# Performance work log

Measured on AMD Instinct MI355X. Metric: run time of the kernel, lower is better.

## Reference

```python
import jax, jax.numpy as jnp
import numpy as np

C, H_HEADS, L_LEV, M_PTS = 256, 4, 3, 4
TAU0 = 1.0


def _ln(x, g, b, eps=1e-5):
    mu = x.mean(-1, keepdims=True)
    var = ((x - mu) ** 2).mean(-1, keepdims=True)
    return (x - mu) * jax.lax.rsqrt(var + eps) * g + b


def _grid_sample(v, grid):
    """Bilinear grid_sample, padding_mode='zeros', align_corners=True.
    v: [B,C,Hin,Win], grid: [B,N,2] (x,y) in [-1,1] -> [B,N,C]"""
    B, Cc, Hin, Win = v.shape
    x = (grid[..., 0] + 1.0) * 0.5 * (Win - 1)
    y = (grid[..., 1] + 1.0) * 0.5 * (Hin - 1)
    x0 = jnp.floor(x); y0 = jnp.floor(y)
    wx1 = x - x0; wy1 = y - y0
    x0i = x0.astype(jnp.int32); y0i = y0.astype(jnp.int32)
    vflat = v.reshape(B, Cc, Hin * Win).transpose(0, 2, 1)  # [B,HW,C]

    def tap(yi, xi, w):
        valid = ((xi >= 0) & (xi < Win) & (yi >= 0) & (yi < Hin)).astype(v.dtype)
        idx = jnp.clip(yi, 0, Hin - 1) * Win + jnp.clip(xi, 0, Win - 1)  # [B,N]
        g = jax.vmap(lambda vf, i: vf[i])(vflat, idx)  # [B,N,C]
        return g * (w * valid)[..., None]

    return (tap(y0i, x0i, (1 - wy1) * (1 - wx1))
            + tap(y0i, x0i + 1, (1 - wy1) * wx1)
            + tap(y0i + 1, x0i, wy1 * (1 - wx1))
            + tap(y0i + 1, x0i + 1, wy1 * wx1))


def setup_inputs() -> dict:
    key = jax.random.key(0)
    ks = jax.random.split(key, 32)
    B, Hq, Wq = 2, 64, 64
    cins = [256, 512, 1024]
    d = {
        'S':  jax.random.normal(ks[0], (B, C, Hq, Wq), jnp.float32),
        'f0': jax.random.normal(ks[1], (B, cins[0], 64, 64), jnp.float32),
        'f1': jax.random.normal(ks[2], (B, cins[1], 32, 32), jnp.float32),
        'f2': jax.random.normal(ks[3], (B, cins[2], 16, 16), jnp.float32),
        'sim': jax.random.uniform(ks[4], (B, 1, Hq, Wq), jnp.float32),
        # 1x1 conv value projections per level
        'vw0': jax.random.normal(ks[5], (C, cins[0]), jnp.float32) * 0.02,
        'vb0': jnp.zeros((C,), jnp.float32),
        'vw1': jax.random.normal(ks[6], (C, cins[1]), jnp.float32) * 0.02,
        'vb1': jnp.zeros((C,), jnp.float32),
        'vw2': jax.random.normal(ks[7], (C, cins[2]), jnp.float32) * 0.02,
        'vb2': jnp.zeros((C,), jnp.float32),
        'q_w': jax.random.normal(ks[8], (C, C), jnp.float32) * 0.02,
        'q_b': jnp.zeros((C,), jnp.float32),
        # offset/weight predictors (non-zero so sampling is nontrivial)
        'off_w': jax.random.normal(ks[9], (H_HEADS * L_LEV * M_PTS * 2, C), jnp.float32) * 0.01,
        'off_b': jnp.zeros((H_HEADS * L_LEV * M_PTS * 2,), jnp.float32),
        'wgt_w': jax.random.normal(ks[10], (H_HEADS * L_LEV * M_PTS, C), jnp.float32) * 0.02,
        'wgt_b': jnp.zeros((H_HEADS * L_LEV * M_PTS,), jnp.float32),
        'out_w': jax.random.normal(ks[11], (C, H_HEADS * C), jnp.float32) * 0.02,
        'out_b': jnp.zeros((C,), jnp.float32),
        'lnq_g': jnp.ones((C,), jnp.float32), 'lnq_b': jnp.zeros((C,), jnp.float32),
        'lno_g': jnp.ones((C,), jnp.float32), 'lno_b': jnp.zeros((C,), jnp.float32),
        'fc1_w': jax.random.normal(ks[12], (4 * C, C), jnp.float32) * 0.02,
        'fc1_b': jnp.zeros((4 * C,), jnp.float32),
        'fc2_w': jax.random.normal(ks[13], (C, 4 * C), jnp.float32) * 0.02,
        'fc2_b': jnp.zeros((C,), jnp.float32),
    }
    return d


def reference(S, f0, f1, f2, sim, vw0, vb0, vw1, vb1, vw2, vb2, q_w, q_b,
              off_w, off_b, wgt_w, wgt_b, out_w, out_b,
              lnq_g, lnq_b, lno_g, lno_b, fc1_w, fc1_b, fc2_w, fc2_b):
    B, Cc, Hq, Wq = S.shape
    Nq = Hq * Wq
    S_seq = S.reshape(B, Cc, Nq).transpose(0, 2, 1)  # [B,Nq,C]
    Q = _ln(S_seq @ q_w.T + q_b, lnq_g, lnq_b)

    # reference points in [0,1], (x,y)
    ys = jnp.linspace(0.5 / Hq, 1 - 0.5 / Hq, Hq)
    xs = jnp.linspace(0.5 / Wq, 1 - 0.5 / Wq, Wq)
    yy, xx = jnp.meshgrid(ys, xs, indexing='ij')
    ref = jnp.stack([xx, yy], axis=-1).reshape(1, Nq, 2)

    feats = [(f0, vw0, vb0), (f1, vw1, vb1), (f2, vw2, vb2)]
    V = [jnp.einsum('bchw,oc->bohw', f, w) + b[None, :, None, None] for f, w, b in feats]

    off = (Q @ off_w.T + off_b).reshape(B, Nq, H_HEADS, L_LEV, M_PTS, 2)
    wts = (Q @ wgt_w.T + wgt_b).reshape(B, Nq, H_HEADS, L_LEV, M_PTS)

    sim2 = sim[:, 0].reshape(B, Nq, 1)
    tau = TAU0 / (sim2 + 0.001)
    wts = wts / tau.reshape(B, Nq, 1, 1, 1)
    wts = jax.nn.softmax(wts.reshape(B, Nq, H_HEADS, L_LEV * M_PTS), axis=-1)
    wts = wts.reshape(B, Nq, H_HEADS, L_LEV, M_PTS)

    acc = jnp.zeros((B, Nq, H_HEADS, Cc), S.dtype)
    for l in range(L_LEV):
        g01 = ref.reshape(1, Nq, 1, 1, 2) + off[:, :, :, l]  # [B,Nq,H,M,2]
        g = jnp.clip(jnp.tanh(g01 * 2.0 - 1.0), -1.0, 1.0)
        samp = _grid_sample(V[l], g.reshape(B, Nq * H_HEADS * M_PTS, 2))
        samp = samp.reshape(B, Nq, H_HEADS, M_PTS, Cc)
        acc = acc + jnp.einsum('bqhmc,bqhm->bqhc', samp, wts[:, :, :, l])

    Y = acc.reshape(B, Nq, H_HEADS * Cc) @ out_w.T + out_b
    Z = _ln(S_seq + Y, lno_g, lno_b)
    h = jax.nn.gelu(Z @ fc1_w.T + fc1_b, approximate=False)
    Z = Z + (h @ fc2_w.T + fc2_b)
    return Z.transpose(0, 2, 1).reshape(B, Cc, Hq, Wq)
```

## Files before the change

kernel.cpp:

```cpp
#include <hip/hip_runtime.h>
#include <hip/hip_bf16.h>
#include <math.h>

#define NQ 4096
#define CC 256

typedef __attribute__((ext_vector_type(8))) short bfrag;
typedef __attribute__((ext_vector_type(4))) float ffrag;

__device__ inline unsigned short f2bf(float x) {
  __hip_bfloat16 h = __float2bfloat16(x);
  return *reinterpret_cast<unsigned short*>(&h);
}

__device__ inline void gload16(const void* g, void* l) {
  __builtin_amdgcn_global_load_lds(
      (const __attribute__((address_space(1))) void*)g,
      (__attribute__((address_space(3))) void*)l, 16, 0, 0);
}

__device__ void tr64(const float* __restrict__ src, float* __restrict__ dstf,
                     unsigned short* __restrict__ dstb, int Cin, int P,
                     int p0, int c0, int b, float (*t)[73]) {
  int tid = threadIdx.x;
  int rx = tid & 15, ry = tid >> 4;
  const float* Sb = src + (size_t)b * Cin * P + p0 + rx * 4;
  #pragma unroll
  for (int i = 0; i < 4; i++) {
    int r = ry + i * 16;
    float4 v = *(const float4*)(Sb + (size_t)(c0 + r) * P);
    t[r][rx * 4 + 0] = v.x; t[r][rx * 4 + 1] = v.y;
    t[r][rx * 4 + 2] = v.z; t[r][rx * 4 + 3] = v.w;
  }
  __syncthreads();
  size_t ob = (size_t)b * P * Cin;
  #pragma unroll
  for (int i = 0; i < 4; i++) {
    int pr = ry + i * 16;
    float x0 = t[rx * 4 + 0][pr], x1 = t[rx * 4 + 1][pr];
    float x2 = t[rx * 4 + 2][pr], x3 = t[rx * 4 + 3][pr];
    size_t idx = ob + (size_t)(p0 + pr) * Cin + c0 + rx * 4;
    if (dstf) { float4 f4 = make_float4(x0, x1, x2, x3); *(float4*)(dstf + idx) = f4; }
    ushort4 u4;
    u4.x = f2bf(x0); u4.y = f2bf(x1); u4.z = f2bf(x2); u4.w = f2bf(x3);
    *(ushort4*)(dstb + idx) = u4;
  }
}

__global__ __launch_bounds__(256)
void prep_all_k(const float* S, const float* f0, const float* f1, const float* f2,
                const float* q_w, const float* off_w, const float* wgt_w,
                const float* vw0, const float* vw1, const float* vw2,
                const float* out_w, const float* fc1_w, const float* fc2_w,
                const float* off_b, const float* wgt_b,
                float* Sseq, unsigned short* Sbf,
                unsigned short* Xf0, unsigned short* Xf1, unsigned short* Xf2,
                unsigned short* q_wb, unsigned short* owb,
                unsigned short* vw0b, unsigned short* vw1b, unsigned short* vw2b,
                unsigned short* out_wb, unsigned short* fc1_wb,
                unsigned short* fc2_wb, float* bias144) {
  __shared__ float t[64][73];
  int bid = blockIdx.x;
  if (bid < 512) {
    int l = bid;
    tr64(S, Sseq, Sbf, 256, 4096, (l & 63) * 64, ((l >> 6) & 3) * 64, l >> 8, t);
  } else if (bid < 1024) {
    int l = bid - 512;
    tr64(f0, nullptr, Xf0, 256, 4096, (l & 63) * 64, ((l >> 6) & 3) * 64, l >> 8, t);
  } else if (bid < 1280) {
    int l = bid - 1024;
    tr64(f1, nullptr, Xf1, 512, 1024, (l & 15) * 64, ((l >> 4) & 7) * 64, l >> 7, t);
  } else if (bid < 1408) {
    int l = bid - 1280;
    tr64(f2, nullptr, Xf2, 1024, 256, (l & 3) * 64, ((l >> 2) & 15) * 64, l >> 6, t);
  } else if (bid < 2688) {
    int i4 = (bid - 1408) * 256 + threadIdx.x;
    const float* src; unsigned short* dst;
    if (i4 < 16384)       { src = q_w;   dst = q_wb; }
    else if (i4 < 32768)  { i4 -= 16384;  src = vw0;   dst = vw0b; }
    else if (i4 < 65536)  { i4 -= 32768;  src = vw1;   dst = vw1b; }
    else if (i4 < 131072) { i4 -= 65536;  src = vw2;   dst = vw2b; }
    else if (i4 < 196608) { i4 -= 131072; src = out_w; dst = out_wb; }
    else if (i4 < 262144) { i4 -= 196608; src = fc1_w; dst = fc1_wb; }
    else                  { i4 -= 262144; src = fc2_w; dst = fc2_wb; }
    float4 v = ((const float4*)src)[i4];
    ushort4 u; u.x = f2bf(v.x); u.y = f2bf(v.y); u.z = f2bf(v.z); u.w = f2bf(v.w);
    ((ushort4*)dst)[i4] = u;
  } else {
    int e = (bid - 2688) * 256 + threadIdx.x;
    float v = (e < 24576) ? off_w[e] : (e < 36864 ? wgt_w[e - 24576] : 0.f);
    owb[e] = f2bf(v);
    if (e < 96) bias144[e] = off_b[e];
    else if (e < 144) bias144[e] = wgt_b[e - 96];
  }
}

template<int BM, int BN, int WM, int WN, int EPI>
__device__ __forceinline__ void gemm_body(
    const unsigned short* __restrict__ A, const unsigned short* __restrict__ B,
    const float* __restrict__ bias, float* __restrict__ outf,
    unsigned short* __restrict__ outb, int N, int K, int ldo,
    const float* __restrict__ Zres, float* __restrict__ outT,
    int m0, int n0, unsigned short* As, unsigned short* Bs) {
  constexpr int MI = BM / (WM * 16), NI = BN / (WN * 16);
  constexpr int TA = BM / 8, TB = BN / 8;
  constexpr int LBM = (BM == 32) ? 5 : (BM == 64) ? 6 : 7;
  constexpr int LBN = (BN == 64) ? 6 : (BN == 128) ? 7 : 8;
  int tid = threadIdx.x, wave = tid >> 6, lane = tid & 63;
  int quad = lane >> 4, l16 = lane & 15;
  int wm = wave / WN, wn = wave % WN;
  const int mbase = wm * (BM / WM), nbase = wn * (BN / WN);

  ffrag acc[MI][NI];
  #pragma unroll
  for (int i = 0; i < MI; i++)
    #pragma unroll
    for (int j = 0; j < NI; j++) acc[i][j] = (ffrag)0.f;

  for (int k0 = 0; k0 < K; k0 += 64) {
    __syncthreads();
    for (int t = wave; t < TA + TB; t += 4) {
      if (t < TA) {
        int s = t * 64 + lane;
        int kc = s >> LBM, r = s & (BM - 1);
        gload16(A + (size_t)(m0 + r) * K + k0 + kc * 8, (char*)As + t * 1024);
      } else {
        int s = (t - TA) * 64 + lane;
        int kc = s >> LBN, r = s & (BN - 1);
        gload16(B + (size_t)(n0 + r) * K + k0 + kc * 8, (char*)Bs + (t - TA) * 1024);
      }
    }
    __syncthreads();
    #pragma unroll
    for (int ks = 0; ks < 2; ks++) {
      bfrag af[MI], bf[NI];
      #pragma unroll
      for (int mi = 0; mi < MI; mi++)
        af[mi] = *(const bfrag*)(As + ((((ks * 4 + quad) << LBM) + mbase + mi * 16 + l16) << 3));
      #pragma unroll
      for (int ni = 0; ni < NI; ni++)
        bf[ni] = *(const bfrag*)(Bs + ((((ks * 4 + quad) << LBN) + nbase + ni * 16 + l16) << 3));
      #pragma unroll
      for (int mi = 0; mi < MI; mi++)
        #pragma unroll
        for (int ni = 0; ni < NI; ni++)
          acc[mi][ni] = __builtin_amdgcn_mfma_f32_16x16x32_bf16(
              af[mi], bf[ni], acc[mi][ni], 0, 0, 0);
    }
  }

  if (EPI == 2) {
    #pragma unroll
    for (int mi = 0; mi < MI; mi++) {
      int mrow = m0 + mbase + mi * 16 + quad * 4;
      int bb = mrow >> 12, q0 = mrow & (NQ - 1);
      #pragma unroll
      for (int ni = 0; ni < NI; ni++) {
        int n = n0 + nbase + ni * 16 + l16;
        float bv = bias[n];
        float4 v;
        v.x = acc[mi][ni][0] + bv + Zres[(size_t)(mrow + 0) * CC + n];
        v.y = acc[mi][ni][1] + bv + Zres[(size_t)(mrow + 1) * CC + n];
        v.z = acc[mi][ni][2] + bv + Zres[(size_t)(mrow + 2) * CC + n];
        v.w = acc[mi][ni][3] + bv + Zres[(size_t)(mrow + 3) * CC + n];
        *(float4*)(outT + ((size_t)(bb * CC + n)) * NQ + q0) = v;
      }
    }
  } else {
    #pragma unroll
    for (int mi = 0; mi < MI; mi++) {
      int mrow = m0 + mbase + mi * 16 + quad * 4;
      #pragma unroll
      for (int ni = 0; ni < NI; ni++) {
        int n = n0 + nbase + ni * 16 + l16;
        if (n < N) {
          float bv = bias[n];
          #pragma unroll
          for (int r = 0; r < 4; r++) {
            float v = acc[mi][ni][r] + bv;
            if (EPI == 1) {
              v = 0.5f * v * (1.f + erff(v * 0.70710678118654752f));
              outb[(size_t)(mrow + r) * ldo + n] = f2bf(v);
            } else if (EPI == 3) {
              outb[(size_t)(mrow + r) * ldo + n] = f2bf(v);
            } else {
              outf[(size_t)(mrow + r) * ldo + n] = v;
            }
          }
        }
      }
    }
  }
}

template<bool RES>
__device__ __forceinline__ void gemm_ln_body(
    const unsigned short* __restrict__ A, const unsigned short* __restrict__ B,
    const float* __restrict__ bias, const float* __restrict__ res,
    float* __restrict__ outf, unsigned short* __restrict__ outb,
    const float* __restrict__ g, const float* __restrict__ be,
    int K, int m0, char* sm) {
  unsigned short* As = (unsigned short*)sm;
  unsigned short* Bs = (unsigned short*)(sm + 4096);
  float* L = (float*)sm;

  int tid = threadIdx.x, wave = tid >> 6, lane = tid & 63;
  int quad = lane >> 4, l16 = lane & 15;

  ffrag acc[2][4];
  #pragma unroll
  for (int i = 0; i < 2; i++)
    #pragma unroll
    for (int j = 0; j < 4; j++) acc[i][j] = (ffrag)0.f;

  for (int k0 = 0; k0 < K; k0 += 64) {
    __syncthreads();
    for (int t = wave; t < 36; t += 4) {
      if (t < 4) {
        int s = t * 64 + lane;
        int kc = s >> 5, r = s & 31;
        gload16(A + (size_t)(m0 + r) * K + k0 + kc * 8, sm + t * 1024);
      } else {
        int s = (t - 4) * 64 + lane;
        int kc = s >> 8, r = s & 255;
        gload16(B + (size_t)r * K + k0 + kc * 8, sm + 4096 + (t - 4) * 1024);
      }
    }
    __syncthreads();
    #pragma unroll
    for (int ks = 0; ks < 2; ks++) {
      bfrag af[2], bf[4];
      #pragma unroll
      for (int mi = 0; mi < 2; mi++)
        af[mi] = *(const bfrag*)(As + ((((ks * 4 + quad) << 5) + mi * 16 + l16) << 3));
      #pragma unroll
      for (int ni = 0; ni < 4; ni++)
        bf[ni] = *(const bfrag*)(Bs + ((((ks * 4 + quad) << 8) + wave * 64 + ni * 16 + l16) << 3));
      #pragma unroll
      for (int mi = 0; mi < 2; mi++)
        #pragma unroll
        for (int ni = 0; ni < 4; ni++)
          acc[mi][ni] = __builtin_amdgcn_mfma_f32_16x16x32_bf16(
              af[mi], bf[ni], acc[mi][ni], 0, 0, 0);
    }
  }
  __syncthreads();

  #pragma unroll
  for (int mi = 0; mi < 2; mi++) {
    int row = mi * 16 + quad * 4;
    #pragma unroll
    for (int ni = 0; ni < 4; ni++) {
      int col = wave * 64 + ni * 16 + l16;
      float bv = bias[col];
      #pragma unroll
      for (int r = 0; r < 4; r++) {
        float v = acc[mi][ni][r] + bv;
        if (RES) v += res[(size_t)(m0 + row + r) * CC + col];
        L[(row + r) * 264 + col] = v;
      }
    }
  }
  __syncthreads();

  int row = tid >> 3, j = tid & 7;
  int seg = ((j + row) & 7) * 32;
  const float* Lr = L + row * 264 + seg;
  float s1 = 0.f, s2 = 0.f;
  #pragma unroll
  for (int i = 0; i < 8; i++) {
    float4 t4 = *(const float4*)(Lr + i * 4);
    s1 += t4.x + t4.y + t4.z + t4.w;
    s2 += t4.x * t4.x + t4.y * t4.y + t4.z * t4.z + t4.w * t4.w;
  }
  #pragma unroll
  for (int o = 1; o < 8; o <<= 1) {
    s1 += __shfl_xor(s1, o);
    s2 += __shfl_xor(s2, o);
  }
  float mu = s1 * (1.f / 256.f);
  float var = s2 * (1.f / 256.f) - mu * mu;
  float rs = rsqrtf(var + 1e-5f);
  int gm = m0 + row;
  #pragma unroll
  for (int i = 0; i < 8; i++) {
    int col = seg + i * 4;
    float4 t4 = *(const float4*)(Lr + i * 4);
    float4 gg = *(const float4*)(g + col);
    float4 bb4 = *(const float4*)(be + col);
    float4 y;
    y.x = (t4.x - mu) * rs * gg.x + bb4.x;
    y.y = (t4.y - mu) * rs * gg.y + bb4.y;
    y.z = (t4.z - mu) * rs * gg.z + bb4.z;
    y.w = (t4.w - mu) * rs * gg.w + bb4.w;
    ushort4 ub;
    ub.x = f2bf(y.x); ub.y = f2bf(y.y); ub.z = f2bf(y.z); ub.w = f2bf(y.w);
    *(ushort4*)(outb + (size_t)gm * CC + col) = ub;
    if (RES) *(float4*)(outf + (size_t)gm * CC + col) = y;
  }
}

__global__ __launch_bounds__(256)
void qv_k(const unsigned short* Sbf, const unsigned short* q_wb, const float* q_b,
          const float* lnq_g, const float* lnq_b, unsigned short* Qbf,
          const unsigned short* Xf0, const unsigned short* Xf1,
          const unsigned short* Xf2, const unsigned short* vw0b,
          const unsigned short* vw1b, const unsigned short* vw2b,
          const float* vb0, const float* vb1, const float* vb2,
          unsigned short* V0b, unsigned short* V1b, unsigned short* V2b) {
  __shared__ __attribute__((aligned(16))) char sm[36864];
  int bid = blockIdx.x;
  if (bid < 256) {
    gemm_ln_body<false>(Sbf, q_wb, q_b, nullptr, nullptr, Qbf,
                        lnq_g, lnq_b, 256, bid * 32, sm);
  } else {
    int lb = bid - 256;
    const unsigned short *A, *B; const float* bias; unsigned short* out; int K;
    if (lb < 256)      { A = Xf0; B = vw0b; bias = vb0; out = V0b; K = 256; }
    else if (lb < 320) { A = Xf1; B = vw1b; bias = vb1; out = V1b; K = 512;  lb -= 256; }
    else               { A = Xf2; B = vw2b; bias = vb2; out = V2b; K = 1024; lb -= 320; }
    int n0 = (lb & 1) * 128, m0 = (lb >> 1) * 64;
    gemm_body<64, 128, 2, 2, 3>(A, B, bias, nullptr, out, 256, K, 256,
                                nullptr, nullptr, m0, n0,
                                (unsigned short*)sm, (unsigned short*)(sm + 8192));
  }
}

__global__ __launch_bounds__(256)
void outln_k(const unsigned short* accbf, const unsigned short* out_wb,
             const float* out_b, const float* Sseq, float* Z,
             unsigned short* Zbf, const float* lno_g, const float* lno_b) {
  __shared__ __attribute__((aligned(16))) char sm[36864];
  gemm_ln_body<true>(accbf, out_wb, out_b, Sseq, Z, Zbf,
                     lno_g, lno_b, 1024, blockIdx.x * 32, sm);
}

__global__ __launch_bounds__(256)
void offwgt_k(const unsigned short* Qbf, const unsigned short* owb,
              const float* bias144, float* offwgt) {
  __shared__ __attribute__((aligned(16))) unsigned short As[4096];
  __shared__ __attribute__((aligned(16))) unsigned short Bs[8192];
  gemm_body<64, 128, 2, 2, 0>(Qbf, owb, bias144, offwgt, nullptr, 144, 256, 144,
                              nullptr, nullptr, blockIdx.y * 64, blockIdx.x * 128, As, Bs);
}

__global__ __launch_bounds__(256)
void fc1_k(const unsigned short* Zbf, const unsigned short* fc1_wb,
           const float* fc1_b, unsigned short* hbf) {
  __shared__ __attribute__((aligned(16))) unsigned short As[8192];
  __shared__ __attribute__((aligned(16))) unsigned short Bs[8192];
  gemm_body<128, 128, 2, 2, 1>(Zbf, fc1_wb, fc1_b, nullptr, hbf, 1024, 256, 1024,
                               nullptr, nullptr, blockIdx.y * 128, blockIdx.x * 128, As, Bs);
}

__global__ __launch_bounds__(256)
void fc2_k(const unsigned short* hbf, const unsigned short* fc2_wb,
           const float* fc2_b, const float* Z, float* outp) {
  __shared__ __attribute__((aligned(16))) unsigned short As[4096];
  __shared__ __attribute__((aligned(16))) unsigned short Bs[4096];
  gemm_body<64, 64, 2, 2, 2>(hbf, fc2_wb, fc2_b, nullptr, nullptr, 256, 1024, 256,
                             Z, outp, blockIdx.y * 64, blockIdx.x * 64, As, Bs);
}

__global__ __launch_bounds__(256)
void sample_k(const float* __restrict__ ow, const float* __restrict__ sim,
              const unsigned short* __restrict__ V0, const unsigned short* __restrict__ V1,
              const unsigned short* __restrict__ V2, unsigned short* __restrict__ acc) {
  int bn = blockIdx.x;
  int q = ((bn & 7) << 10) | (bn >> 3);
  int b = q >> 12, n = q & (NQ - 1);
  int tid = threadIdx.x, head = tid >> 6, lane = tid & 63;

  __shared__ float s_w[48];
  __shared__ int   s_xy[48][2];
  __shared__ float s_f[48][2];
  __shared__ int   s_off[192];
  __shared__ float s_twt[192];

  if (tid < 48) {
    int hh = tid / 12, pt = tid % 12, l = pt >> 2, mm = pt & 3;
    int oidx = (hh * 3 + l) * 4 + mm;
    float offx = ow[(size_t)q * 144 + oidx * 2 + 0];
    float offy = ow[(size_t)q * 144 + oidx * 2 + 1];
    float refx = ((n & 63) + 0.5f) * (1.f / 64.f);
    float refy = ((n >> 6) + 0.5f) * (1.f / 64.f);
    float gx = tanhf((refx + offx) * 2.f - 1.f);
    float gy = tanhf((refy + offy) * 2.f - 1.f);
    gx = fminf(1.f, fmaxf(-1.f, gx));
    gy = fminf(1.f, fmaxf(-1.f, gy));
    int Wl = 64 >> l;
    float x = (gx + 1.f) * 0.5f * (float)(Wl - 1);
    float y = (gy + 1.f) * 0.5f * (float)(Wl - 1);
    float x0 = floorf(x), y0 = floorf(y);
    s_xy[tid][0] = (int)x0;
    s_xy[tid][1] = (int)y0;
    s_f[tid][0] = x - x0;
    s_f[tid][1] = y - y0;
    s_w[tid] = ow[(size_t)q * 144 + 96 + oidx] * (sim[q] + 0.001f);
  }
  __syncthreads();
  if (tid < 4) {
    float mx = -1e30f;
    #pragma unroll
    for (int i = 0; i < 12; i++) mx = fmaxf(mx, s_w[tid * 12 + i]);
    float e[12], ssum = 0.f;
    #pragma unroll
    for (int i = 0; i < 12; i++) { e[i] = expf(s_w[tid * 12 + i] - mx); ssum += e[i]; }
    float inv = 1.f / ssum;
    #pragma unroll
    for (int i = 0; i < 12; i++) s_w[tid * 12 + i] = e[i] * inv;
  }
  __syncthreads();
  if (tid < 192) {
    int s = tid >> 2, tap = tid & 3;
    int l = (s % 12) >> 2;
    int Wl = 64 >> l;
    int X = s_xy[s][0] + (tap & 1), Y = s_xy[s][1] + (tap >> 1);
    bool valid = (X >= 0 && X < Wl && Y >= 0 && Y < Wl);
    float wx = (tap & 1) ? s_f[s][0] : 1.f - s_f[s][0];
    float wy = (tap >> 1) ? s_f[s][1] : 1.f - s_f[s][1];
    s_twt[tid] = valid ? s_w[s] * wx * wy : 0.f;
    int Xc = min(max(X, 0), Wl - 1), Yc = min(max(Y, 0), Wl - 1);
    s_off[tid] = (Yc * Wl + Xc) << 8;
  }
  __syncthreads();

  const unsigned short* B0 = V0 + (size_t)b * 4096 * CC;
  const unsigned short* B1 = V1 + (size_t)b * 1024 * CC;
  const unsigned short* B2 = V2 + (size_t)b * 256 * CC;
  int lane4 = lane * 4;
  float4 a = make_float4(0.f, 0.f, 0.f, 0.f);
  #pragma unroll
  for (int pt = 0; pt < 12; pt++) {
    const unsigned short* base = (pt < 4) ? B0 : (pt < 8) ? B1 : B2;
    int s = head * 12 + pt;
    #pragma unroll
    for (int tap = 0; tap < 4; tap++) {
      int off = s_off[s * 4 + tap];
      float w = s_twt[s * 4 + tap];
      const uint2 u = *(const uint2*)(base + off + lane4);
      a.x = fmaf(w, __uint_as_float(u.x << 16), a.x);
      a.y = fmaf(w, __uint_as_float(u.x & 0xffff0000u), a.y);
      a.z = fmaf(w, __uint_as_float(u.y << 16), a.z);
      a.w = fmaf(w, __uint_as_float(u.y & 0xffff0000u), a.w);
    }
  }
  ushort4 r;
  r.x = f2bf(a.x); r.y = f2bf(a.y); r.z = f2bf(a.z); r.w = f2bf(a.w);
  *(ushort4*)(acc + (size_t)q * 1024 + head * CC + lane4) = r;
}

extern "C" void kernel_launch(void* const* d_in, const int* in_sizes, int n_in,
                              void* d_out, int out_size, void* d_ws, size_t ws_size,
                              hipStream_t stream) {
  const float* S     = (const float*)d_in[0];
  const float* f0    = (const float*)d_in[1];
  const float* f1    = (const float*)d_in[2];
  const float* f2    = (const float*)d_in[3];
  const float* sim   = (const float*)d_in[4];
  const float* vw0   = (const float*)d_in[5];
  const float* vb0   = (const float*)d_in[6];
  const float* vw1   = (const float*)d_in[7];
  const float* vb1   = (const float*)d_in[8];
  const float* vw2   = (const float*)d_in[9];
  const float* vb2   = (const float*)d_in[10];
  const float* q_w   = (const float*)d_in[11];
  const float* q_b   = (const float*)d_in[12];
  const float* off_w = (const float*)d_in[13];
  const float* off_b = (const float*)d_in[14];
  const float* wgt_w = (const float*)d_in[15];
  const float* wgt_b = (const float*)d_in[16];
  const float* out_w = (const float*)d_in[17];
  const float* out_b = (const float*)d_in[18];
  const float* lnq_g = (const float*)d_in[19];
  const float* lnq_b = (const float*)d_in[20];
  const float* lno_g = (const float*)d_in[21];
  const float* lno_b = (const float*)d_in[22];
  const float* fc1_w = (const float*)d_in[23];
  const float* fc1_b = (const float*)d_in[24];
  const float* fc2_w = (const float*)d_in[25];
  const float* fc2_b = (const float*)d_in[26];

  char* p = (char*)d_ws;
  float* Sseq   = (float*)p; p += 8388608;
  float* Z      = (float*)p; p += 8388608;
  float* offwgt = (float*)p; p += 4718592;
  float* bias144 = (float*)p; p += 1024;
  unsigned short* Sbf   = (unsigned short*)p; p += 4194304;
  unsigned short* Qbf   = (unsigned short*)p; p += 4194304;
  unsigned short* accbf = (unsigned short*)p; p += 16777216;
  unsigned short* V0b   = (unsigned short*)p; p += 4194304;
  unsigned short* V1b   = (unsigned short*)p; p += 1048576;
  unsigned short* V2b   = (unsigned short*)p; p += 262144;
  unsigned short* q_wb   = (unsigned short*)p; p += 131072;
  unsigned short* owb    = (unsigned short*)p; p += 131072;
  unsigned short* vw0b   = (unsigned short*)p; p += 131072;
  unsigned short* vw1b   = (unsigned short*)p; p += 262144;
  unsigned short* vw2b   = (unsigned short*)p; p += 524288;
  unsigned short* out_wb = (unsigned short*)p; p += 524288;
  unsigned short* fc1_wb = (unsigned short*)p; p += 524288;
  unsigned short* fc2_wb = (unsigned short*)p; p += 524288;

  unsigned short* Xf0 = accbf;
  unsigned short* Xf1 = accbf + 2097152;
  unsigned short* Xf2 = accbf + 3145728;
  unsigned short* Zbf = Qbf;
  unsigned short* hbf = accbf;
  float* outp = (float*)d_out;

  prep_all_k<<<2944, 256, 0, stream>>>(S, f0, f1, f2, q_w, off_w, wgt_w,
      vw0, vw1, vw2, out_w, fc1_w, fc2_w, off_b, wgt_b,
      Sseq, Sbf, Xf0, Xf1, Xf2, q_wb, owb, vw0b, vw1b, vw2b, out_wb,
      fc1_wb, fc2_wb, bias144);

  qv_k<<<592, 256, 0, stream>>>(Sbf, q_wb, q_b, lnq_g, lnq_b, Qbf,
      Xf0, Xf1, Xf2, vw0b, vw1b, vw2b, vb0, vb1, vb2, V0b, V1b, V2b);

  offwgt_k<<<dim3(2, 128), 256, 0, stream>>>(Qbf, owb, bias144, offwgt);

  sample_k<<<8192, 256, 0, stream>>>(offwgt, sim, V0b, V1b, V2b, accbf);

  outln_k<<<256, 256, 0, stream>>>(accbf, out_wb, out_b, Sseq, Z, Zbf,
      lno_g, lno_b);

  fc1_k<<<dim3(8, 64), 256, 0, stream>>>(Zbf, fc1_wb, fc1_b, hbf);

  fc2_k<<<dim3(4, 128), 256, 0, stream>>>(hbf, fc2_wb, fc2_b, Z, outp);
}
```

Measured before the change: 296.1 us.

## Drop fp32 transposed S copy and widen sampler gathers to 16-byte loads

The prep kernel no longer writes a transposed fp32 copy of S. The out-projection LayerNorm epilogue now reads the residual straight from the original channel-major S layout with float4 loads across four consecutive queries. Separately, the sampling kernel has each half-wave gather 8 bf16 channels per tap with uint4 loads, splitting the taps between halves and combining them with a cross-half shuffle. This cuts per-lane load count and packs offset and weight into one LDS entry. The trade-off is strided residual reads in the epilogue and an extra shuffle reduction in the sampler.

```diff
diff --git a/kernel.cpp b/kernel.cpp
--- a/kernel.cpp
+++ b/kernel.cpp
@@ -19,7 +19,7 @@
       (__attribute__((address_space(3))) void*)l, 16, 0, 0);
 }
 
-__device__ void tr64(const float* __restrict__ src, float* __restrict__ dstf,
+__device__ void tr64(const float* __restrict__ src,
                      unsigned short* __restrict__ dstb, int Cin, int P,
                      int p0, int c0, int b, float (*t)[73]) {
   int tid = threadIdx.x;
@@ -40,7 +40,6 @@
     float x0 = t[rx * 4 + 0][pr], x1 = t[rx * 4 + 1][pr];
     float x2 = t[rx * 4 + 2][pr], x3 = t[rx * 4 + 3][pr];
     size_t idx = ob + (size_t)(p0 + pr) * Cin + c0 + rx * 4;
-    if (dstf) { float4 f4 = make_float4(x0, x1, x2, x3); *(float4*)(dstf + idx) = f4; }
     ushort4 u4;
     u4.x = f2bf(x0); u4.y = f2bf(x1); u4.z = f2bf(x2); u4.w = f2bf(x3);
     *(ushort4*)(dstb + idx) = u4;
@@ -53,7 +52,7 @@
                 const float* vw0, const float* vw1, const float* vw2,
                 const float* out_w, const float* fc1_w, const float* fc2_w,
                 const float* off_b, const float* wgt_b,
-                float* Sseq, unsigned short* Sbf,
+                unsigned short* Sbf,
                 unsigned short* Xf0, unsigned short* Xf1, unsigned short* Xf2,
                 unsigned short* q_wb, unsigned short* owb,
                 unsigned short* vw0b, unsigned short* vw1b, unsigned short* vw2b,
@@ -63,16 +62,16 @@
   int bid = blockIdx.x;
   if (bid < 512) {
     int l = bid;
-    tr64(S, Sseq, Sbf, 256, 4096, (l & 63) * 64, ((l >> 6) & 3) * 64, l >> 8, t);
+    tr64(S, Sbf, 256, 4096, (l & 63) * 64, ((l >> 6) & 3) * 64, l >> 8, t);
   } else if (bid < 1024) {
     int l = bid - 512;
-    tr64(f0, nullptr, Xf0, 256, 4096, (l & 63) * 64, ((l >> 6) & 3) * 64, l >> 8, t);
+    tr64(f0, Xf0, 256, 4096, (l & 63) * 64, ((l >> 6) & 3) * 64, l >> 8, t);
   } else if (bid < 1280) {
     int l = bid - 1024;
-    tr64(f1, nullptr, Xf1, 512, 1024, (l & 15) * 64, ((l >> 4) & 7) * 64, l >> 7, t);
+    tr64(f1, Xf1, 512, 1024, (l & 15) * 64, ((l >> 4) & 7) * 64, l >> 7, t);
   } else if (bid < 1408) {
     int l = bid - 1280;
-    tr64(f2, nullptr, Xf2, 1024, 256, (l & 3) * 64, ((l >> 2) & 15) * 64, l >> 6, t);
+    tr64(f2, Xf2, 1024, 256, (l & 3) * 64, ((l >> 2) & 15) * 64, l >> 6, t);
   } else if (bid < 2688) {
     int i4 = (bid - 1408) * 256 + threadIdx.x;
     const float* src; unsigned short* dst;
@@ -196,7 +195,7 @@
 template<bool RES>
 __device__ __forceinline__ void gemm_ln_body(
     const unsigned short* __restrict__ A, const unsigned short* __restrict__ B,
-    const float* __restrict__ bias, const float* __restrict__ res,
+    const float* __restrict__ bias, const float* __restrict__ Sraw,
     float* __restrict__ outf, unsigned short* __restrict__ outb,
     const float* __restrict__ g, const float* __restrict__ be,
     int K, int m0, char* sm) {
@@ -249,16 +248,18 @@
   #pragma unroll
   for (int mi = 0; mi < 2; mi++) {
     int row = mi * 16 + quad * 4;
+    int m = m0 + row;
+    int bb = m >> 12, q0 = m & (NQ - 1);
     #pragma unroll
     for (int ni = 0; ni < 4; ni++) {
       int col = wave * 64 + ni * 16 + l16;
       float bv = bias[col];
-      #pragma unroll
-      for (int r = 0; r < 4; r++) {
-        float v = acc[mi][ni][r] + bv;
-        if (RES) v += res[(size_t)(m0 + row + r) * CC + col];
-        L[(row + r) * 264 + col] = v;
-      }
+      float4 s4 = make_float4(0.f, 0.f, 0.f, 0.f);
+      if (RES) s4 = *(const float4*)(Sraw + ((size_t)(bb * CC + col)) * NQ + q0);
+      L[(row + 0) * 264 + col] = acc[mi][ni][0] + bv + s4.x;
+      L[(row + 1) * 264 + col] = acc[mi][ni][1] + bv + s4.y;
+      L[(row + 2) * 264 + col] = acc[mi][ni][2] + bv + s4.z;
+      L[(row + 3) * 264 + col] = acc[mi][ni][3] + bv + s4.w;
     }
   }
   __syncthreads();
@@ -328,10 +329,10 @@
 
 __global__ __launch_bounds__(256)
 void outln_k(const unsigned short* accbf, const unsigned short* out_wb,
-             const float* out_b, const float* Sseq, float* Z,
+             const float* out_b, const float* S, float* Z,
              unsigned short* Zbf, const float* lno_g, const float* lno_b) {
   __shared__ __attribute__((aligned(16))) char sm[36864];
-  gemm_ln_body<true>(accbf, out_wb, out_b, Sseq, Z, Zbf,
+  gemm_ln_body<true>(accbf, out_wb, out_b, S, Z, Zbf,
                      lno_g, lno_b, 1024, blockIdx.x * 32, sm);
 }
 
@@ -370,12 +371,12 @@
   int q = ((bn & 7) << 10) | (bn >> 3);
   int b = q >> 12, n = q & (NQ - 1);
   int tid = threadIdx.x, head = tid >> 6, lane = tid & 63;
+  int half = lane >> 5, l32 = lane & 31;
 
   __shared__ float s_w[48];
   __shared__ int   s_xy[48][2];
   __shared__ float s_f[48][2];
-  __shared__ int   s_off[192];
-  __shared__ float s_twt[192];
+  __shared__ uint2 s_ow[192];
 
   if (tid < 48) {
     int hh = tid / 12, pt = tid % 12, l = pt >> 2, mm = pt & 3;
@@ -419,35 +420,46 @@
     bool valid = (X >= 0 && X < Wl && Y >= 0 && Y < Wl);
     float wx = (tap & 1) ? s_f[s][0] : 1.f - s_f[s][0];
     float wy = (tap >> 1) ? s_f[s][1] : 1.f - s_f[s][1];
-    s_twt[tid] = valid ? s_w[s] * wx * wy : 0.f;
+    float twt = valid ? s_w[s] * wx * wy : 0.f;
     int Xc = min(max(X, 0), Wl - 1), Yc = min(max(Y, 0), Wl - 1);
-    s_off[tid] = (Yc * Wl + Xc) << 8;
+    s_ow[tid].x = (unsigned)((Yc * Wl + Xc) << 8);
+    s_ow[tid].y = __float_as_uint(twt);
   }
   __syncthreads();
 
   const unsigned short* B0 = V0 + (size_t)b * 4096 * CC;
   const unsigned short* B1 = V1 + (size_t)b * 1024 * CC;
   const unsigned short* B2 = V2 + (size_t)b * 256 * CC;
-  int lane4 = lane * 4;
-  float4 a = make_float4(0.f, 0.f, 0.f, 0.f);
-  #pragma unroll
-  for (int pt = 0; pt < 12; pt++) {
-    const unsigned short* base = (pt < 4) ? B0 : (pt < 8) ? B1 : B2;
-    int s = head * 12 + pt;
-    #pragma unroll
-    for (int tap = 0; tap < 4; tap++) {
-      int off = s_off[s * 4 + tap];
-      float w = s_twt[s * 4 + tap];
-      const uint2 u = *(const uint2*)(base + off + lane4);
-      a.x = fmaf(w, __uint_as_float(u.x << 16), a.x);
-      a.y = fmaf(w, __uint_as_float(u.x & 0xffff0000u), a.y);
-      a.z = fmaf(w, __uint_as_float(u.y << 16), a.z);
-      a.w = fmaf(w, __uint_as_float(u.y & 0xffff0000u), a.w);
-    }
-  }
-  ushort4 r;
-  r.x = f2bf(a.x); r.y = f2bf(a.y); r.z = f2bf(a.z); r.w = f2bf(a.w);
-  *(ushort4*)(acc + (size_t)q * 1024 + head * CC + lane4) = r;
+  int ch8 = l32 * 8;
+  float a0 = 0.f, a1 = 0.f, a2 = 0.f, a3 = 0.f;
+  float a4 = 0.f, a5 = 0.f, a6 = 0.f, a7 = 0.f;
+  #pragma unroll
+  for (int it = 0; it < 24; it++) {
+    const unsigned short* base = (it < 8) ? B0 : (it < 16) ? B1 : B2;
+    uint2 owv = s_ow[head * 48 + it * 2 + half];
+    float w = __uint_as_float(owv.y);
+    const uint4 u = *(const uint4*)(base + owv.x + ch8);
+    a0 = fmaf(w, __uint_as_float(u.x << 16), a0);
+    a1 = fmaf(w, __uint_as_float(u.x & 0xffff0000u), a1);
+    a2 = fmaf(w, __uint_as_float(u.y << 16), a2);
+    a3 = fmaf(w, __uint_as_float(u.y & 0xffff0000u), a3);
+    a4 = fmaf(w, __uint_as_float(u.z << 16), a4);
+    a5 = fmaf(w, __uint_as_float(u.z & 0xffff0000u), a5);
+    a6 = fmaf(w, __uint_as_float(u.w << 16), a6);
+    a7 = fmaf(w, __uint_as_float(u.w & 0xffff0000u), a7);
+  }
+  a0 += __shfl_xor(a0, 32); a1 += __shfl_xor(a1, 32);
+  a2 += __shfl_xor(a2, 32); a3 += __shfl_xor(a3, 32);
+  a4 += __shfl_xor(a4, 32); a5 += __shfl_xor(a5, 32);
+  a6 += __shfl_xor(a6, 32); a7 += __shfl_xor(a7, 32);
+  if (half == 0) {
+    uint4 r;
+    r.x = (unsigned)f2bf(a0) | ((unsigned)f2bf(a1) << 16);
+    r.y = (unsigned)f2bf(a2) | ((unsigned)f2bf(a3) << 16);
+    r.z = (unsigned)f2bf(a4) | ((unsigned)f2bf(a5) << 16);
+    r.w = (unsigned)f2bf(a6) | ((unsigned)f2bf(a7) << 16);
+    *(uint4*)(acc + (size_t)q * 1024 + head * CC + ch8) = r;
+  }
 }
 
 extern "C" void kernel_launch(void* const* d_in, const int* in_sizes, int n_in,
@@ -482,7 +494,6 @@
   const float* fc2_b = (const float*)d_in[26];
 
   char* p = (char*)d_ws;
-  float* Sseq   = (float*)p; p += 8388608;
   float* Z      = (float*)p; p += 8388608;
   float* offwgt = (float*)p; p += 4718592;
   float* bias144 = (float*)p; p += 1024;
@@ -510,7 +521,7 @@
 
   prep_all_k<<<2944, 256, 0, stream>>>(S, f0, f1, f2, q_w, off_w, wgt_w,
       vw0, vw1, vw2, out_w, fc1_w, fc2_w, off_b, wgt_b,
-      Sseq, Sbf, Xf0, Xf1, Xf2, q_wb, owb, vw0b, vw1b, vw2b, out_wb,
+      Sbf, Xf0, Xf1, Xf2, q_wb, owb, vw0b, vw1b, vw2b, out_wb,
       fc1_wb, fc2_wb, bias144);
 
   qv_k<<<592, 256, 0, stream>>>(Sbf, q_wb, q_b, lnq_g, lnq_b, Qbf,
@@ -520,7 +531,7 @@
 
   sample_k<<<8192, 256, 0, stream>>>(offwgt, sim, V0b, V1b, V2b, accbf);
 
-  outln_k<<<256, 256, 0, stream>>>(accbf, out_wb, out_b, Sseq, Z, Zbf,
+  outln_k<<<256, 256, 0, stream>>>(accbf, out_wb, out_b, S, Z, Zbf,
       lno_g, lno_b);
 
   fc1_k<<<dim3(8, 64), 256, 0, stream>>>(Zbf, fc1_wb, fc1_b, hbf);
```

Measured after the change: 276.3 us. 1.07x faster.
